# Kernel tuning notes

Hardware: AMD Instinct MI355X
Metric: run time of the kernel (lower is better)

The kernel has to match this reference:

```python
import jax, jax.numpy as jnp
import numpy as np

B, S, HID = 1, 2048, 2880
H, HKV, D = 64, 8, 64
WINDOW = 128
SCALE = D ** -0.5
NEG = -1e30


def _rope(x, cos, sin):
    # x: [B, S, h, D]; cos/sin: [S, D//2]; interleaved complex rotation
    x1 = x[..., 0::2]
    x2 = x[..., 1::2]
    c = cos[None, :, None, :]
    s = sin[None, :, None, :]
    o1 = x1 * c - x2 * s
    o2 = x1 * s + x2 * c
    out = jnp.stack([o1, o2], axis=-1)  # [B,S,h,D/2,2]
    return out.reshape(x.shape)


def setup_inputs() -> dict:
    key = jax.random.key(0)
    ks = jax.random.split(key, 12)
    x = jax.random.normal(ks[0], (B, S, HID), dtype=jnp.float32)
    # rotary tables (head_dim/2 frequencies)
    inv_freq = 1.0 / (10000.0 ** (np.arange(0, D, 2, dtype=np.float32) / D))
    t = np.arange(S, dtype=np.float32)
    ang = np.outer(t, inv_freq)  # [S, D/2]
    cos = jnp.asarray(np.cos(ang))
    sin = jnp.asarray(np.sin(ang))
    std = 0.02
    Wq = jax.random.normal(ks[1], (HID, H * D), dtype=jnp.float32) * std
    bq = jnp.zeros((H * D,), dtype=jnp.float32)
    Wk = jax.random.normal(ks[2], (HID, HKV * D), dtype=jnp.float32) * std
    bk = jnp.zeros((HKV * D,), dtype=jnp.float32)
    Wv = jax.random.normal(ks[3], (HID, HKV * D), dtype=jnp.float32) * std
    bv = jnp.zeros((HKV * D,), dtype=jnp.float32)
    Wo = jax.random.normal(ks[4], (H * D, HID), dtype=jnp.float32) * std
    bo = jnp.zeros((HID,), dtype=jnp.float32)
    sinks = jax.random.normal(ks[5], (H,), dtype=jnp.float32) * std
    return {"x": x, "cos": cos, "sin": sin, "Wq": Wq, "bq": bq,
            "Wk": Wk, "bk": bk, "Wv": Wv, "bv": bv, "Wo": Wo, "bo": bo,
            "sinks": sinks}


def reference(x, cos, sin, Wq, bq, Wk, bk, Wv, bv, Wo, bo, sinks):
    b, s, _ = x.shape
    q = (x @ Wq + bq).reshape(b, s, H, D)
    k = (x @ Wk + bk).reshape(b, s, HKV, D)
    v = (x @ Wv + bv).reshape(b, s, HKV, D)
    q = _rope(q, cos, sin)
    k = _rope(k, cos, sin)
    # GQA: expand kv heads to H
    rep = H // HKV
    k = jnp.repeat(k, rep, axis=2)  # [B,S,H,D]
    v = jnp.repeat(v, rep, axis=2)
    scores = jnp.einsum("bqhd,bkhd->bhqk", q, k) * SCALE  # [B,H,S,S]
    i = jnp.arange(s)[:, None]
    j = jnp.arange(s)[None, :]
    mask = (j <= i) & (i - j < WINDOW)  # causal sliding window
    z = jnp.where(mask[None, None], scores, NEG)
    sink = sinks[None, :, None]  # [1,H,1] extra logit per head
    m = jnp.maximum(jnp.max(z, axis=-1), sink)  # [B,H,S]
    p = jnp.exp(z - m[..., None])
    denom = jnp.sum(p, axis=-1) + jnp.exp(sink - m)  # [B,H,S]
    out = jnp.einsum("bhqk,bkhd->bhqd", p, v) / denom[..., None]
    out = out.transpose(0, 2, 1, 3).reshape(b, s, H * D)
    return out @ Wo + bo
```

## Files before the change

### kernel.cpp

```cpp
#include <hip/hip_runtime.h>
#include <stdint.h>

#define S_LEN   2048
#define HID_DIM 2880
#define NHEAD   64
#define NKVH    8
#define DHEAD   64
#define NQ      4096
#define NKVD    512
#define NQKV    5120
#define WOPAD   2944
#define ATT_SCALE 0.125f
#define NEGINF  (-1e30f)

typedef __attribute__((ext_vector_type(8))) short bf16x8;
typedef __attribute__((ext_vector_type(4))) float f32x4;

typedef __attribute__((address_space(3))) uint32_t lds_u32;
typedef const __attribute__((address_space(1))) uint32_t glb_u32;

__device__ __forceinline__ void gl_lds16(const short* g, short* l) {
  __builtin_amdgcn_global_load_lds((glb_u32*)(uintptr_t)g,
                                   (lds_u32*)(uint32_t)(uintptr_t)l, 16, 0, 0);
}

__device__ __forceinline__ short f2bf(float f) {
  union { float f; uint32_t u; } c; c.f = f;
  uint32_t u = c.u;
  return (short)((u + 0x7FFFu + ((u >> 16) & 1u)) >> 16);
}

__global__ __launch_bounds__(256) void k_prep(
    const float* __restrict__ x, short* __restrict__ xb,
    const float* __restrict__ Wq, const float* __restrict__ Wk,
    const float* __restrict__ Wv, const float* __restrict__ Wo,
    short* __restrict__ wqkvb, short* __restrict__ wob) {
  int b = blockIdx.x;
  if (b < 5760) {
    int i = b * 256 + threadIdx.x;
    float4 v = ((const float4*)x)[i];
    short4 o;
    o.x = f2bf(v.x); o.y = f2bf(v.y); o.z = f2bf(v.z); o.w = f2bf(v.w);
    ((short4*)xb)[i] = o;
    return;
  }
  b -= 5760;
  const float* src; short* dst; int K, N, tk;
  if (b < 11520) {
    src = Wq; dst = wqkvb; K = 2880; N = 4096; tk = 90;
  } else if (b < 11520 + 1440) {
    b -= 11520;
    src = Wk; dst = wqkvb + (size_t)NQ * HID_DIM; K = 2880; N = 512; tk = 90;
  } else if (b < 11520 + 2880) {
    b -= 11520 + 1440;
    src = Wv; dst = wqkvb + (size_t)(NQ + NKVD) * HID_DIM; K = 2880; N = 512; tk = 90;
  } else {
    b -= 11520 + 2880;
    src = Wo; dst = wob; K = 4096; N = 2880; tk = 128;
  }
  int k0 = (b % tk) * 32, n0 = (b / tk) * 32;
  __shared__ float tile[32][33];
  int tx = threadIdx.x & 31, ty = threadIdx.x >> 5;
#pragma unroll
  for (int j = 0; j < 4; ++j) {
    int n = n0 + tx, k = k0 + ty + j * 8;
    tile[ty + j * 8][tx] = (n < N) ? src[(size_t)k * N + n] : 0.f;
  }
  __syncthreads();
#pragma unroll
  for (int j = 0; j < 4; ++j) {
    int n = n0 + ty + j * 8;
    dst[(size_t)n * K + k0 + tx] = f2bf(tile[tx][ty + j * 8]);
  }
}

template <int EPI>
__global__ __launch_bounds__(512) void k_gemm(
    const short* __restrict__ A, const short* __restrict__ B, int K,
    const float* __restrict__ biasq, const float* __restrict__ biask,
    const float* __restrict__ biasv,
    const float* __restrict__ cosT, const float* __restrict__ sinT,
    short* __restrict__ qout, short* __restrict__ kout, short* __restrict__ vout,
    const float* __restrict__ bo, float* __restrict__ out) {
  const int tid = threadIdx.x;
  const int lane = tid & 63, wid = tid >> 6;
  const int wm = wid >> 2, wn = wid & 3;
  const int l15 = lane & 15, lhi = lane >> 4;
  const int row0 = blockIdx.y * 128, col0 = blockIdx.x * 128;

  __shared__ short As[128 * 64];
  __shared__ short Bs[128 * 64];

  f32x4 acc[4][2];
#pragma unroll
  for (int i = 0; i < 4; ++i)
#pragma unroll
    for (int j = 0; j < 2; ++j) acc[i][j] = (f32x4){0.f, 0.f, 0.f, 0.f};

  const short* aSrc[2];
  const short* bSrc[2];
  int dOff[2];
#pragma unroll
  for (int i = 0; i < 2; ++i) {
    int p = i * 512 + tid;
    int m = p >> 3, slot = p & 7;
    int ss = slot ^ (m & 7);
    aSrc[i] = A + (size_t)(row0 + m) * K + ss * 8;
    bSrc[i] = B + (size_t)(col0 + m) * K + ss * 8;
    dOff[i] = p * 8;
  }

  const int nkt = K >> 6;
  for (int kt = 0; kt < nkt; ++kt) {
    __syncthreads();
#pragma unroll
    for (int i = 0; i < 2; ++i) gl_lds16(aSrc[i] + kt * 64, &As[dOff[i]]);
#pragma unroll
    for (int i = 0; i < 2; ++i) gl_lds16(bSrc[i] + kt * 64, &Bs[dOff[i]]);
    __syncthreads();
#pragma unroll
    for (int kk = 0; kk < 2; ++kk) {
      bf16x8 af[4], bf[2];
#pragma unroll
      for (int mi = 0; mi < 4; ++mi) {
        int r = wm * 64 + mi * 16 + l15;
        int sl = (kk * 4 + lhi) ^ (r & 7);
        af[mi] = *(const bf16x8*)((char*)As + r * 128 + sl * 16);
      }
#pragma unroll
      for (int ni = 0; ni < 2; ++ni) {
        int r = wn * 32 + ni * 16 + l15;
        int sl = (kk * 4 + lhi) ^ (r & 7);
        bf[ni] = *(const bf16x8*)((char*)Bs + r * 128 + sl * 16);
      }
#pragma unroll
      for (int mi = 0; mi < 4; ++mi)
#pragma unroll
        for (int ni = 0; ni < 2; ++ni)
          acc[mi][ni] = __builtin_amdgcn_mfma_f32_16x16x32_bf16(af[mi], bf[ni], acc[mi][ni], 0, 0, 0);
    }
  }

  if (EPI == 0) {
#pragma unroll
    for (int mi = 0; mi < 4; ++mi) {
#pragma unroll
      for (int r = 0; r < 4; ++r) {
        int mg = row0 + wm * 64 + mi * 16 + lhi * 4 + r;
#pragma unroll
        for (int ni = 0; ni < 2; ++ni) {
          int ng = col0 + wn * 32 + ni * 16 + l15;
          float v = acc[mi][ni][r];
          v += (ng < NQ) ? biasq[ng] : (ng < NQ + NKVD ? biask[ng - NQ] : biasv[ng - NQ - NKVD]);
          if (ng < NQ + NKVD) {
            float partner = __shfl_xor(v, 1);
            int d = ng & 63, p = d >> 1;
            float c = cosT[mg * 32 + p], s = sinT[mg * 32 + p];
            v = (d & 1) ? (partner * s + v * c) : (v * c - partner * s);
          }
          short b16 = f2bf(v);
          if (ng < NQ)              qout[(size_t)mg * NQ + ng] = b16;
          else if (ng < NQ + NKVD)  kout[(size_t)mg * NKVD + (ng - NQ)] = b16;
          else                      vout[(size_t)mg * NKVD + (ng - NQ - NKVD)] = b16;
        }
      }
    }
  } else {
#pragma unroll
    for (int mi = 0; mi < 4; ++mi) {
#pragma unroll
      for (int r = 0; r < 4; ++r) {
        int mg = row0 + wm * 64 + mi * 16 + lhi * 4 + r;
#pragma unroll
        for (int ni = 0; ni < 2; ++ni) {
          int ng = col0 + wn * 32 + ni * 16 + l15;
          if (ng < HID_DIM) out[(size_t)mg * HID_DIM + ng] = acc[mi][ni][r] + bo[ng];
        }
      }
    }
  }
}

__global__ __launch_bounds__(256) void k_attn(
    const short* __restrict__ qb, const short* __restrict__ kb,
    const short* __restrict__ vb, const float* __restrict__ sinks,
    short* __restrict__ attnb) {
  const int h = blockIdx.x & 63;
  const int q0 = (blockIdx.x >> 6) * 64;
  const int tid = threadIdx.x;
  const int lane = tid & 63, wq = tid >> 6;
  const int l15 = lane & 15, lhi = lane >> 4;
  const int hkv = h >> 3;
  const int kstart = q0 - 128;

  __shared__ short Vt[64 * 256];
  __shared__ short Plds[4][16 * 168];

  {
    int d = tid >> 2;
    int k16 = (tid & 3) * 16;
#pragma unroll
    for (int j = 0; j < 16; j += 4)
      *(short4*)&Vt[d * 256 + 192 + k16 + j] = (short4){0, 0, 0, 0};
  }

  {
    int krow = tid >> 2;
    int dbase = (tid & 3) * 16;
#pragma unroll
    for (int rep = 0; rep < 3; ++rep) {
      int key = rep * 64 + krow;
      int gk = kstart + key;
      int gkc = gk < 0 ? 0 : gk;
      const short* src = vb + (size_t)gkc * NKVD + hkv * 64 + dbase;
      uint4 v0 = *(const uint4*)(src);
      uint4 v1 = *(const uint4*)(src + 8);
      uint32_t w[8] = {v0.x, v0.y, v0.z, v0.w, v1.x, v1.y, v1.z, v1.w};
#pragma unroll
      for (int i = 0; i < 8; ++i) {
        int d0 = dbase + 2 * i, d1 = dbase + 2 * i + 1;
        Vt[d0 * 256 + (key ^ ((d0 & 7) << 3))] = (short)(w[i] & 0xffffu);
        Vt[d1 * 256 + (key ^ ((d1 & 7) << 3))] = (short)(w[i] >> 16);
      }
    }
  }

  int qrow = q0 + wq * 16 + l15;
  bf16x8 aq[2];
#pragma unroll
  for (int kk = 0; kk < 2; ++kk)
    aq[kk] = *(const bf16x8*)(qb + (size_t)qrow * NQ + h * 64 + kk * 32 + lhi * 8);

  f32x4 sacc[9];
#pragma unroll
  for (int ni = 0; ni < 9; ++ni) {
    int key = kstart + (wq + ni) * 16 + l15;
    int keyc = key < 0 ? 0 : key;
    const short* kp = kb + (size_t)keyc * NKVD + hkv * 64;
    bf16x8 b0 = *(const bf16x8*)(kp + lhi * 8);
    bf16x8 b1 = *(const bf16x8*)(kp + 32 + lhi * 8);
    f32x4 z = (f32x4){0.f, 0.f, 0.f, 0.f};
    z = __builtin_amdgcn_mfma_f32_16x16x32_bf16(aq[0], b0, z, 0, 0, 0);
    z = __builtin_amdgcn_mfma_f32_16x16x32_bf16(aq[1], b1, z, 0, 0, 0);
    sacc[ni] = z;
  }

  float snk = sinks[h];
  float mx[4] = {NEGINF, NEGINF, NEGINF, NEGINF};
#pragma unroll
  for (int ni = 0; ni < 9; ++ni) {
    int j = kstart + (wq + ni) * 16 + l15;
#pragma unroll
    for (int r = 0; r < 4; ++r) {
      int iq = q0 + wq * 16 + lhi * 4 + r;
      float sv = sacc[ni][r] * ATT_SCALE;
      bool valid = (j >= 0) && (j <= iq) && (iq - j < 128);
      sv = valid ? sv : NEGINF;
      sacc[ni][r] = sv;
      mx[r] = fmaxf(mx[r], sv);
    }
  }
#pragma unroll
  for (int r = 0; r < 4; ++r) {
    float m = mx[r];
    m = fmaxf(m, __shfl_xor(m, 1));
    m = fmaxf(m, __shfl_xor(m, 2));
    m = fmaxf(m, __shfl_xor(m, 4));
    m = fmaxf(m, __shfl_xor(m, 8));
    mx[r] = fmaxf(m, snk);
  }
  float sm[4] = {0.f, 0.f, 0.f, 0.f};
#pragma unroll
  for (int ni = 0; ni < 9; ++ni)
#pragma unroll
    for (int r = 0; r < 4; ++r) {
      float p = __expf(sacc[ni][r] - mx[r]);
      sacc[ni][r] = p;
      sm[r] += p;
    }
  float inv[4];
#pragma unroll
  for (int r = 0; r < 4; ++r) {
    float s = sm[r];
    s += __shfl_xor(s, 1);
    s += __shfl_xor(s, 2);
    s += __shfl_xor(s, 4);
    s += __shfl_xor(s, 8);
    s += __expf(snk - mx[r]);
    inv[r] = 1.0f / s;
  }

  short* pw = &Plds[wq][0];
#pragma unroll
  for (int ni = 0; ni < 9; ++ni)
#pragma unroll
    for (int r = 0; r < 4; ++r)
      pw[(lhi * 4 + r) * 168 + ni * 16 + l15] = f2bf(sacc[ni][r]);
#pragma unroll
  for (int r = 0; r < 4; ++r)
    pw[(lhi * 4 + r) * 168 + 144 + l15] = 0;

  __syncthreads();

  f32x4 oacc[4];
#pragma unroll
  for (int nt = 0; nt < 4; ++nt) oacc[nt] = (f32x4){0.f, 0.f, 0.f, 0.f};
  const short* pr = &Plds[wq][0];
#pragma unroll
  for (int ks = 0; ks < 5; ++ks) {
    bf16x8 pf = *(const bf16x8*)(pr + l15 * 168 + ks * 32 + lhi * 8);
#pragma unroll
    for (int nt = 0; nt < 4; ++nt) {
      int d = nt * 16 + l15;
      int keyidx = wq * 16 + ks * 32 + lhi * 8;
      bf16x8 vf = *(const bf16x8*)(&Vt[d * 256 + (keyidx ^ ((d & 7) << 3))]);
      oacc[nt] = __builtin_amdgcn_mfma_f32_16x16x32_bf16(pf, vf, oacc[nt], 0, 0, 0);
    }
  }

#pragma unroll
  for (int nt = 0; nt < 4; ++nt)
#pragma unroll
    for (int r = 0; r < 4; ++r) {
      int iq = q0 + wq * 16 + lhi * 4 + r;
      int d = nt * 16 + l15;
      attnb[(size_t)iq * NQ + h * 64 + d] = f2bf(oacc[nt][r] * inv[r]);
    }
}

extern "C" void kernel_launch(void* const* d_in, const int* in_sizes, int n_in,
                              void* d_out, int out_size, void* d_ws, size_t ws_size,
                              hipStream_t stream) {
  const float* x     = (const float*)d_in[0];
  const float* cosT  = (const float*)d_in[1];
  const float* sinT  = (const float*)d_in[2];
  const float* Wq    = (const float*)d_in[3];
  const float* bq    = (const float*)d_in[4];
  const float* Wk    = (const float*)d_in[5];
  const float* bk    = (const float*)d_in[6];
  const float* Wv    = (const float*)d_in[7];
  const float* bv    = (const float*)d_in[8];
  const float* Wo    = (const float*)d_in[9];
  const float* bo    = (const float*)d_in[10];
  const float* sinks = (const float*)d_in[11];
  float* out = (float*)d_out;

  short* xb    = (short*)d_ws;
  short* wqkvb = xb + (size_t)S_LEN * HID_DIM;
  short* wob   = wqkvb + (size_t)NQKV * HID_DIM;
  short* qbuf  = wob + (size_t)WOPAD * NQ;
  short* kbuf  = qbuf + (size_t)S_LEN * NQ;
  short* vbuf  = kbuf + (size_t)S_LEN * NKVD;
  short* attnb = vbuf + (size_t)S_LEN * NKVD;

  k_prep<<<31936, 256, 0, stream>>>(x, xb, Wq, Wk, Wv, Wo, wqkvb, wob);

  k_gemm<0><<<dim3(NQKV / 128, S_LEN / 128), 512, 0, stream>>>(
      xb, wqkvb, HID_DIM, bq, bk, bv, cosT, sinT, qbuf, kbuf, vbuf, nullptr, nullptr);

  k_attn<<<(S_LEN / 64) * NHEAD, 256, 0, stream>>>(qbuf, kbuf, vbuf, sinks, attnb);

  k_gemm<1><<<dim3(WOPAD / 128, S_LEN / 128), 512, 0, stream>>>(
      attnb, wob, NQ, nullptr, nullptr, nullptr, nullptr, nullptr,
      nullptr, nullptr, nullptr, bo, out);
}
```

Measured before the change: 224.3 us.

## Split-K the output projection GEMM into two halves with a reduce kernel

The output projection GEMM now launches with a z-dimension of two, and each slice computes half of the K=4096 reduction. Each slice writes bf16 partial sums into a scratch buffer that reuses the x bf16 workspace. A new reduce kernel adds the two partials and the bias and writes fp32 output. This doubles the block count of the previously small 23x16 grid to improve CU occupancy, at the cost of an extra kernel launch, extra memory traffic, and bf16 rounding of the partial sums.

```diff
diff --git a/kernel.cpp b/kernel.cpp
--- a/kernel.cpp
+++ b/kernel.cpp
@@ -28,6 +28,11 @@
   union { float f; uint32_t u; } c; c.f = f;
   uint32_t u = c.u;
   return (short)((u + 0x7FFFu + ((u >> 16) & 1u)) >> 16);
+}
+
+__device__ __forceinline__ float bf2f(short s) {
+  union { uint32_t u; float f; } c; c.u = ((uint32_t)(uint16_t)s) << 16;
+  return c.f;
 }
 
 __global__ __launch_bounds__(256) void k_prep(
@@ -81,12 +86,14 @@
     const float* __restrict__ biasv,
     const float* __restrict__ cosT, const float* __restrict__ sinT,
     short* __restrict__ qout, short* __restrict__ kout, short* __restrict__ vout,
-    const float* __restrict__ bo, float* __restrict__ out) {
+    short* __restrict__ pbuf) {
   const int tid = threadIdx.x;
   const int lane = tid & 63, wid = tid >> 6;
   const int wm = wid >> 2, wn = wid & 3;
   const int l15 = lane & 15, lhi = lane >> 4;
   const int row0 = blockIdx.y * 128, col0 = blockIdx.x * 128;
+  const int kOff = (EPI == 1) ? blockIdx.z * 2048 : 0;
+  const int nkt = (EPI == 1) ? 32 : (K >> 6);
 
   __shared__ short As[128 * 64];
   __shared__ short Bs[128 * 64];
@@ -105,12 +112,11 @@
     int p = i * 512 + tid;
     int m = p >> 3, slot = p & 7;
     int ss = slot ^ (m & 7);
-    aSrc[i] = A + (size_t)(row0 + m) * K + ss * 8;
-    bSrc[i] = B + (size_t)(col0 + m) * K + ss * 8;
+    aSrc[i] = A + (size_t)(row0 + m) * K + kOff + ss * 8;
+    bSrc[i] = B + (size_t)(col0 + m) * K + kOff + ss * 8;
     dOff[i] = p * 8;
   }
 
-  const int nkt = K >> 6;
   for (int kt = 0; kt < nkt; ++kt) {
     __syncthreads();
 #pragma unroll
@@ -166,6 +172,7 @@
       }
     }
   } else {
+    short* pd = pbuf + (size_t)blockIdx.z * ((size_t)S_LEN * WOPAD);
 #pragma unroll
     for (int mi = 0; mi < 4; ++mi) {
 #pragma unroll
@@ -174,11 +181,36 @@
 #pragma unroll
         for (int ni = 0; ni < 2; ++ni) {
           int ng = col0 + wn * 32 + ni * 16 + l15;
-          if (ng < HID_DIM) out[(size_t)mg * HID_DIM + ng] = acc[mi][ni][r] + bo[ng];
+          pd[(size_t)mg * WOPAD + ng] = f2bf(acc[mi][ni][r]);
         }
       }
     }
   }
+}
+
+__global__ __launch_bounds__(256) void k_reduce(
+    const short* __restrict__ pbuf, const float* __restrict__ bo,
+    float* __restrict__ out) {
+  int idx = (blockIdx.x * 256 + threadIdx.x) * 8;
+  int mg = idx / HID_DIM, ng = idx % HID_DIM;
+  const short* p0 = pbuf + (size_t)mg * WOPAD + ng;
+  const short* p1 = p0 + (size_t)S_LEN * WOPAD;
+  uint4 a = *(const uint4*)p0;
+  uint4 b = *(const uint4*)p1;
+  float4 ob0 = *(const float4*)(bo + ng);
+  float4 ob1 = *(const float4*)(bo + ng + 4);
+  const uint32_t* aw = (const uint32_t*)&a;
+  const uint32_t* bw = (const uint32_t*)&b;
+  float o[8];
+#pragma unroll
+  for (int j = 0; j < 4; ++j) {
+    o[2 * j]     = bf2f((short)(aw[j] & 0xffffu)) + bf2f((short)(bw[j] & 0xffffu));
+    o[2 * j + 1] = bf2f((short)(aw[j] >> 16))     + bf2f((short)(bw[j] >> 16));
+  }
+  float4 r0 = (float4){o[0] + ob0.x, o[1] + ob0.y, o[2] + ob0.z, o[3] + ob0.w};
+  float4 r1 = (float4){o[4] + ob1.x, o[5] + ob1.y, o[6] + ob1.z, o[7] + ob1.w};
+  *(float4*)(out + (size_t)mg * HID_DIM + ng) = r0;
+  *(float4*)(out + (size_t)mg * HID_DIM + ng + 4) = r1;
 }
 
 __global__ __launch_bounds__(256) void k_attn(
@@ -352,15 +384,18 @@
   short* kbuf  = qbuf + (size_t)S_LEN * NQ;
   short* vbuf  = kbuf + (size_t)S_LEN * NKVD;
   short* attnb = vbuf + (size_t)S_LEN * NKVD;
+  short* pbuf  = xb;
 
   k_prep<<<31936, 256, 0, stream>>>(x, xb, Wq, Wk, Wv, Wo, wqkvb, wob);
 
   k_gemm<0><<<dim3(NQKV / 128, S_LEN / 128), 512, 0, stream>>>(
-      xb, wqkvb, HID_DIM, bq, bk, bv, cosT, sinT, qbuf, kbuf, vbuf, nullptr, nullptr);
+      xb, wqkvb, HID_DIM, bq, bk, bv, cosT, sinT, qbuf, kbuf, vbuf, nullptr);
 
   k_attn<<<(S_LEN / 64) * NHEAD, 256, 0, stream>>>(qbuf, kbuf, vbuf, sinks, attnb);
 
-  k_gemm<1><<<dim3(WOPAD / 128, S_LEN / 128), 512, 0, stream>>>(
+  k_gemm<1><<<dim3(WOPAD / 128, S_LEN / 128, 2), 512, 0, stream>>>(
       attnb, wob, NQ, nullptr, nullptr, nullptr, nullptr, nullptr,
-      nullptr, nullptr, nullptr, bo, out);
-}
+      nullptr, nullptr, nullptr, pbuf);
+
+  k_reduce<<<S_LEN * HID_DIM / (256 * 8), 256, 0, stream>>>(pbuf, bo, out);
+}
```

New measurement: 231.3 us. 1.03x slower.
